# Kernel tuning notes

Hardware: AMD Instinct MI355X
Metric: run time of the kernel (lower is better)

Reference implementation:

```python
import jax, jax.numpy as jnp
import numpy as np

B, T_MEL, F_BINS, C = 32, 1024, 4, 256
S_PHONES = 256
MAX_DUR = 8


def setup_inputs() -> dict:
    key = jax.random.key(0)
    k1, k2 = jax.random.split(key)
    e_src = jax.random.normal(k1, (B, T_MEL, F_BINS, C), dtype=jnp.float32)
    d_src = jax.random.randint(k2, (B, S_PHONES), 0, MAX_DUR, dtype=jnp.int64)
    return {"e_src": e_src, "d_src": d_src}


def reference(e_src, d_src):
    # e_src: [B, T, F, C] prosody features; d_src: [B, S] phone durations (frames).
    # Original: agg[b, i] = mean over dims (0,1) of e_src[b, start_i:start_i+d_i],
    # i.e. mean over (frames_of_phone_i, freq); zeros if the slice is empty.
    Bd, T, Fb, Cd = e_src.shape
    S = d_src.shape[1]
    x = e_src.mean(axis=2)  # [B, T, C] mean over freq (uniform, commutes with frame mean)
    cum = jnp.cumsum(d_src, axis=1)  # [B, S] phone boundary ends
    t = jnp.arange(T)
    # frame -> phone id; frames beyond total duration go to dump segment S
    sid = jax.vmap(lambda c: jnp.searchsorted(c, t, side="right"))(cum)  # [B, T]

    def per_utt(xi, si):
        ssum = jax.ops.segment_sum(xi, si, num_segments=S + 1)[:S]  # [S, C]
        cnt = jax.ops.segment_sum(jnp.ones((T,), xi.dtype), si, num_segments=S + 1)[:S]
        return ssum, cnt

    seg_sum, counts = jax.vmap(per_utt)(x, sid)  # [B,S,C], [B,S]
    mean = seg_sum / jnp.maximum(counts, 1.0)[..., None]
    return jnp.where(counts[..., None] > 0, mean, jnp.zeros((), x.dtype))
```

## Files before the change

### kernel.cpp

```cpp
#include <hip/hip_runtime.h>


#define NB 32
#define NT 1024
#define NF 4
#define NC 256
#define NS 256

__global__ __launch_bounds__(256) void FastSpeech2Pros_83769042141888_kernel(
    const float* __restrict__ e_src,
    const int*   __restrict__ d_src,
    float*       __restrict__ out)
{
    const int s = blockIdx.x;
    const int b = blockIdx.y;
    const int t = threadIdx.x;

    __shared__ int cs[NS];
    cs[t] = d_src[b * NS + t];
    __syncthreads();
    #pragma unroll
    for (int off = 1; off < NS; off <<= 1) {
        int v = (t >= off) ? cs[t - off] : 0;
        __syncthreads();
        cs[t] += v;
        __syncthreads();
    }

    int end   = cs[s];
    int start = (s == 0) ? 0 : cs[s - 1];
    if (start > NT) start = NT;
    if (end   > NT) end   = NT;
    const int cnt = end - start;

    float4 acc = make_float4(0.f, 0.f, 0.f, 0.f);
    const float4* base =
        (const float4*)(e_src + (size_t)b * NT * NF * NC);
    for (int fr = start; fr < end; ++fr) {
        float4 v = base[(size_t)fr * (NF * NC / 4) + t];
        acc.x += v.x; acc.y += v.y; acc.z += v.z; acc.w += v.w;
    }

    __shared__ float4 red[256];
    red[t] = acc;
    __syncthreads();

    if (t < 64) {
        float4 a0 = red[t];
        float4 a1 = red[t + 64];
        float4 a2 = red[t + 128];
        float4 a3 = red[t + 192];
        const float inv = (cnt > 0) ? (1.0f / (4.0f * (float)cnt)) : 0.0f;
        float4 o;
        o.x = (a0.x + a1.x + a2.x + a3.x) * inv;
        o.y = (a0.y + a1.y + a2.y + a3.y) * inv;
        o.z = (a0.z + a1.z + a2.z + a3.z) * inv;
        o.w = (a0.w + a1.w + a2.w + a3.w) * inv;
        ((float4*)(out + ((size_t)b * NS + s) * NC))[t] = o;
    }
}

extern "C" void kernel_launch(void* const* d_in, const int* in_sizes, int n_in,
                              void* d_out, int out_size, void* d_ws, size_t ws_size,
                              hipStream_t stream) {
    const float* e_src = (const float*)d_in[0];
    const int*   d_src = (const int*)d_in[1];
    float*       out   = (float*)d_out;

    dim3 grid(NS, NB);
    FastSpeech2Pros_83769042141888_kernel<<<grid, 256, 0, stream>>>(e_src, d_src, out);
}
```

Baseline: 187.8 us.

## Split prefix scan into separate kernel and map one wave per segment

The duration prefix scan moves into its own small kernel that runs once per utterance and writes (start, end) pairs to workspace. Before this, every (segment, batch) block redid the full 256-wide scan with repeated barriers. The mean kernel now gives each 64-lane wave one segment and has each lane accumulate all four frequency bins itself, which removes the shared-memory reduction and its barrier. The cost is an extra kernel launch and a small workspace round trip.

```diff
diff --git a/kernel.cpp b/kernel.cpp
--- a/kernel.cpp
+++ b/kernel.cpp
@@ -7,13 +7,11 @@
 #define NC 256
 #define NS 256
 
-__global__ __launch_bounds__(256) void FastSpeech2Pros_83769042141888_kernel(
-    const float* __restrict__ e_src,
-    const int*   __restrict__ d_src,
-    float*       __restrict__ out)
+__global__ __launch_bounds__(256) void fs2_scan_kernel(
+    const int* __restrict__ d_src,
+    int2*      __restrict__ se)
 {
-    const int s = blockIdx.x;
-    const int b = blockIdx.y;
+    const int b = blockIdx.x;
     const int t = threadIdx.x;
 
     __shared__ int cs[NS];
@@ -27,37 +25,44 @@
         __syncthreads();
     }
 
-    int end   = cs[s];
-    int start = (s == 0) ? 0 : cs[s - 1];
+    int end   = cs[t];
+    int start = (t == 0) ? 0 : cs[t - 1];
     if (start > NT) start = NT;
     if (end   > NT) end   = NT;
-    const int cnt = end - start;
+    se[b * NS + t] = make_int2(start, end);
+}
+
+__global__ __launch_bounds__(256) void fs2_segmean_kernel(
+    const float* __restrict__ e_src,
+    const int2*  __restrict__ se,
+    float*       __restrict__ out)
+{
+    const int wave = threadIdx.x >> 6;
+    const int lane = threadIdx.x & 63;
+    const int s    = blockIdx.x * 4 + wave;
+    const int b    = blockIdx.y;
+
+    const int2 r    = se[b * NS + s];
+    const int start = r.x;
+    const int end   = r.y;
+
+    const float4* base = (const float4*)(e_src + (size_t)b * NT * NF * NC);
 
     float4 acc = make_float4(0.f, 0.f, 0.f, 0.f);
-    const float4* base =
-        (const float4*)(e_src + (size_t)b * NT * NF * NC);
     for (int fr = start; fr < end; ++fr) {
-        float4 v = base[(size_t)fr * (NF * NC / 4) + t];
-        acc.x += v.x; acc.y += v.y; acc.z += v.z; acc.w += v.w;
+        const float4* fb = base + (size_t)fr * (NF * NC / 4);
+        #pragma unroll
+        for (int f = 0; f < NF; ++f) {
+            float4 v = fb[f * 64 + lane];
+            acc.x += v.x; acc.y += v.y; acc.z += v.z; acc.w += v.w;
+        }
     }
 
-    __shared__ float4 red[256];
-    red[t] = acc;
-    __syncthreads();
-
-    if (t < 64) {
-        float4 a0 = red[t];
-        float4 a1 = red[t + 64];
-        float4 a2 = red[t + 128];
-        float4 a3 = red[t + 192];
-        const float inv = (cnt > 0) ? (1.0f / (4.0f * (float)cnt)) : 0.0f;
-        float4 o;
-        o.x = (a0.x + a1.x + a2.x + a3.x) * inv;
-        o.y = (a0.y + a1.y + a2.y + a3.y) * inv;
-        o.z = (a0.z + a1.z + a2.z + a3.z) * inv;
-        o.w = (a0.w + a1.w + a2.w + a3.w) * inv;
-        ((float4*)(out + ((size_t)b * NS + s) * NC))[t] = o;
-    }
+    const int cnt = end - start;
+    const float inv = (cnt > 0) ? (1.0f / (4.0f * (float)cnt)) : 0.0f;
+    float4 o;
+    o.x = acc.x * inv; o.y = acc.y * inv; o.z = acc.z * inv; o.w = acc.w * inv;
+    ((float4*)(out + ((size_t)b * NS + s) * NC))[lane] = o;
 }
 
 extern "C" void kernel_launch(void* const* d_in, const int* in_sizes, int n_in,
@@ -66,7 +71,10 @@
     const float* e_src = (const float*)d_in[0];
     const int*   d_src = (const int*)d_in[1];
     float*       out   = (float*)d_out;
+    int2*        se    = (int2*)d_ws;
 
-    dim3 grid(NS, NB);
-    FastSpeech2Pros_83769042141888_kernel<<<grid, 256, 0, stream>>>(e_src, d_src, out);
+    fs2_scan_kernel<<<NB, NS, 0, stream>>>(d_src, se);
+
+    dim3 grid(NS / 4, NB);
+    fs2_segmean_kernel<<<grid, 256, 0, stream>>>(e_src, se, out);
 }
```

Measured after the change: 192.7 us. 2.6% more time.
